# Optimization experiments

Hardware: AMD Instinct MI355X
Metric: run time of the kernel (lower is better)

Reference implementation:

```python
import jax, jax.numpy as jnp
import numpy as np

N_NODES = 100000
N_FEATS = 256
OUT_DIM = 64
NNZ_X = 1280000
N_EDGES = 1600000
KEEP_PROB = 0.9  # 1 - dropout_rate (dropout_rate = 0.1)


def setup_inputs() -> dict:
    key = jax.random.key(0)
    ks = jax.random.split(key, 7)
    feat_values = jax.random.normal(ks[0], (NNZ_X,), dtype=jnp.float32)
    feat_rows = jax.random.randint(ks[1], (NNZ_X,), 0, N_NODES, dtype=jnp.int32)
    feat_cols = jax.random.randint(ks[2], (NNZ_X,), 0, N_FEATS, dtype=jnp.int32)
    # GlorotNormal kernel: std = sqrt(2 / (fan_in + fan_out))
    glorot_std = float(np.sqrt(2.0 / (N_FEATS + OUT_DIM)))
    kernel = jax.random.normal(ks[3], (N_FEATS, OUT_DIM), dtype=jnp.float32) * glorot_std
    adj_values = jax.random.uniform(ks[4], (N_EDGES,), dtype=jnp.float32)
    adj_rows = jax.random.randint(ks[5], (N_EDGES,), 0, N_NODES, dtype=jnp.int32)
    adj_cols = jax.random.randint(ks[6], (N_EDGES,), 0, N_NODES, dtype=jnp.int32)
    return {
        "feat_values": feat_values,
        "kernel": kernel,
        "adj_values": adj_values,
        "feat_rows": feat_rows,
        "feat_cols": feat_cols,
        "adj_rows": adj_rows,
        "adj_cols": adj_cols,
    }


def reference(feat_values, kernel, adj_values, feat_rows, feat_cols, adj_rows, adj_cols):
    # sparse dropout on feature values (training=True path), deterministic key.
    # tf: keep = floor(keep_prob + U[0,1)) cast to bool; retain then scale 1/keep_prob
    u = jax.random.uniform(jax.random.key(42), feat_values.shape, dtype=feat_values.dtype)
    keep = jnp.floor(KEEP_PROB + u).astype(bool)
    v = jnp.where(keep, feat_values, jnp.zeros_like(feat_values)) * (1.0 / KEEP_PROB)

    # SpMM 1: XW[n, o] = sum_{(n,f) in X} v * kernel[f, o]
    xw = jax.ops.segment_sum(v[:, None] * kernel[feat_cols], feat_rows,
                             num_segments=N_NODES)  # [N, OUT]

    # SpMM 2: out[i, o] = sum_{(i,j) in A} a_ij * xw[j, o]
    agg = jax.ops.segment_sum(adj_values[:, None] * xw[adj_cols], adj_rows,
                              num_segments=N_NODES)  # [N, OUT]

    return jax.nn.relu(agg)
```

## Files before the change

kernel.cpp:

```cpp
#include <hip/hip_runtime.h>

#define N_NODES 100000
#define N_FEATS 256
#define OUT_DIM 64
#define NNZ_X   1280000
#define N_EDGES 1600000
#define NB      391
#define CHUNK   4096
#define KPT     8
#define CAPX    4352
#define CAPA    5120

__device__ __forceinline__ unsigned rotl32(unsigned x, unsigned d) {
    return (x << d) | (x >> (32u - d));
}

__device__ __forceinline__ float jax_uniform_42(unsigned e) {
    unsigned x0 = 0u, x1 = e;
    const unsigned ks0 = 0u, ks1 = 42u, ks2 = 0u ^ 42u ^ 0x1BD11BDAu;
    x0 += ks0; x1 += ks1;
#define TF_R(r) { x0 += x1; x1 = rotl32(x1, r); x1 ^= x0; }
    TF_R(13) TF_R(15) TF_R(26) TF_R(6)
    x0 += ks1; x1 += ks2 + 1u;
    TF_R(17) TF_R(29) TF_R(16) TF_R(24)
    x0 += ks2; x1 += ks0 + 2u;
    TF_R(13) TF_R(15) TF_R(26) TF_R(6)
    x0 += ks0; x1 += ks1 + 3u;
    TF_R(17) TF_R(29) TF_R(16) TF_R(24)
    x0 += ks1; x1 += ks2 + 4u;
    TF_R(13) TF_R(15) TF_R(26) TF_R(6)
    x0 += ks2; x1 += ks0 + 5u;
#undef TF_R
    unsigned bits = x0 ^ x1;
    return __uint_as_float((bits >> 9) | 0x3f800000u) - 1.0f;
}

__device__ __forceinline__ bool keep_42(unsigned e) {
    float u = jax_uniform_42(e);
    return floorf(0.9f + u) != 0.0f;
}

__device__ __forceinline__ unsigned short f32_bf16(float f) {
    unsigned bits = __float_as_uint(f);
    return (unsigned short)((bits + 0x7fffu + ((bits >> 16) & 1u)) >> 16);
}

__device__ __forceinline__ float bf16_f32(unsigned short u) {
    return __uint_as_float((unsigned)u << 16);
}

__global__ __launch_bounds__(512) void phase1(
        const float* __restrict__ fvals, const int* __restrict__ frows,
        const int* __restrict__ fcols,
        const float* __restrict__ avals, const int* __restrict__ arows,
        const int* __restrict__ acols,
        int* __restrict__ bcur_x, int* __restrict__ bcur_a,
        float2* __restrict__ gx, float2* __restrict__ ga) {
    const int isA = blockIdx.y;
    const float* vals = isA ? avals : fvals;
    const int* rows   = isA ? arows : frows;
    const int* cols   = isA ? acols : fcols;
    int* bcur         = isA ? bcur_a : bcur_x;
    float2* dst       = isA ? ga : gx;
    const unsigned cap = isA ? CAPA : CAPX;
    const unsigned n  = isA ? N_EDGES : NNZ_X;

    unsigned t = threadIdx.x;
    unsigned base = blockIdx.x * CHUNK;
    if (base >= n) return;

    __shared__ int cnt[512];
    __shared__ int start[512];
    __shared__ int cur[512];
    __shared__ int gbase[NB];
    __shared__ int s[256];
    __shared__ unsigned pArr[CHUNK];

    int rcache[KPT];

    cnt[t] = 0;
    __syncthreads();
    #pragma unroll
    for (int k = 0; k < KPT; k++) {
        unsigned i = base + k * 512u + t;
        int r = -1;
        if (i < n) {
            int rr = rows[i];
            if (isA || keep_42(i)) r = rr;
        }
        rcache[k] = r;
        if (r >= 0) atomicAdd(&cnt[(unsigned)r >> 8], 1);
    }
    __syncthreads();
    if (t < 256) s[t] = cnt[2*t] + cnt[2*t+1];
    __syncthreads();
    for (int off = 1; off < 256; off <<= 1) {
        int v = (t < 256u && t >= (unsigned)off) ? s[t - off] : 0;
        __syncthreads();
        if (t < 256u) s[t] += v;
        __syncthreads();
    }
    if (t < 256u) {
        int excl = t ? s[t-1] : 0;
        start[2*t]   = excl;
        start[2*t+1] = excl + cnt[2*t];
        cur[2*t]     = excl;
        cur[2*t+1]   = excl + cnt[2*t];
    }
    for (unsigned b = t; b < NB; b += 512u) {
        int cb = cnt[b];
        if (cb > 0) gbase[b] = atomicAdd(&bcur[b], cb);
    }
    __syncthreads();
    int n_valid = s[255];
    #pragma unroll
    for (int k = 0; k < KPT; k++) {
        int r = rcache[k];
        if (r >= 0) {
            unsigned b = (unsigned)r >> 8;
            int p = atomicAdd(&cur[b], 1);
            pArr[p] = (b << 20) | (((unsigned)r & 255u) << 12) | (k * 512u + t);
        }
    }
    __syncthreads();
    #pragma unroll
    for (int k = 0; k < KPT; k++) {
        int sidx = k * 512 + (int)t;
        if (sidx < n_valid) {
            unsigned m = pArr[sidx];
            unsigned b = m >> 20;
            unsigned rowlow = (m >> 12) & 255u;
            unsigned i = base + (m & 4095u);
            float v = vals[i];
            if (!isA) v *= (float)(1.0 / 0.9);
            unsigned packed = ((unsigned)cols[i] << 8) | rowlow;
            float2 e; e.x = v; e.y = __int_as_float((int)packed);
            dst[(size_t)b * cap + gbase[b] + (sidx - start[b])] = e;
        }
    }
}

__global__ __launch_bounds__(512) void sort_stage(
        const int* __restrict__ bcur_x, const float2* __restrict__ gx,
        const float* __restrict__ W, unsigned short* __restrict__ xw,
        const int* __restrict__ bcur_a, float2* __restrict__ ga,
        unsigned short* __restrict__ rs) {
    __shared__ float2 ent[CAPX];
    __shared__ int hist[256];
    __shared__ int starts[256];
    __shared__ int cursor[256];
    __shared__ int wtot[4];
    unsigned t = threadIdx.x;
    unsigned wid = t >> 6, lane = t & 63u;
    const int isA = (blockIdx.x >= NB);
    unsigned b = isA ? (blockIdx.x - NB) : blockIdx.x;

    if (!isA) {
        int cnt = bcur_x[b];
        const float2* src = gx + (size_t)b * CAPX;
        if (t < 256) hist[t] = 0;
        __syncthreads();
        for (int i = (int)t; i < cnt; i += 512)
            atomicAdd(&hist[((unsigned)__float_as_int(src[i].y)) & 255u], 1);
        __syncthreads();
        int inc = 0, binv = 0;
        if (wid < 4u) {
            unsigned bin = wid * 64u + lane;
            binv = hist[bin];
            inc = binv;
            #pragma unroll
            for (int d = 1; d < 64; d <<= 1) {
                int v = __shfl_up(inc, d, 64);
                if (lane >= (unsigned)d) inc += v;
            }
            if (lane == 63u) wtot[wid] = inc;
        }
        __syncthreads();
        if (wid < 4u) {
            int offw = 0;
            #pragma unroll
            for (int w = 0; w < 4; w++) if ((unsigned)w < wid) offw += wtot[w];
            unsigned bin = wid * 64u + lane;
            int excl = inc - binv + offw;
            starts[bin] = excl;
            cursor[bin] = excl;
        }
        __syncthreads();
        for (int i = (int)t; i < cnt; i += 512) {
            float2 e = src[i];
            int pos = atomicAdd(&cursor[((unsigned)__float_as_int(e.y)) & 255u], 1);
            ent[pos] = e;
        }
        __syncthreads();
        unsigned quarter = lane >> 4, sub = lane & 15u;
        const float4* W4 = (const float4*)W;
        ushort4* xw4 = (ushort4*)xw;
        for (unsigned r = wid; r < 256u; r += 8u) {
            int s0 = starts[r];
            int s1 = (r == 255u) ? cnt : starts[r + 1];
            float4 acc[4];
            #pragma unroll
            for (int j = 0; j < 4; j++) { acc[j].x = acc[j].y = acc[j].z = acc[j].w = 0.0f; }
            int p = s0;
            for (; p + 16 <= s1; p += 16) {
                float2 e[4];
                #pragma unroll
                for (int j = 0; j < 4; j++) e[j] = ent[p + 4 * quarter + j];
                float4 w[4];
                #pragma unroll
                for (int j = 0; j < 4; j++)
                    w[j] = W4[(((unsigned)__float_as_int(e[j].y)) >> 8) * 16u + sub];
                #pragma unroll
                for (int j = 0; j < 4; j++) {
                    acc[j].x = fmaf(e[j].x, w[j].x, acc[j].x);
                    acc[j].y = fmaf(e[j].x, w[j].y, acc[j].y);
                    acc[j].z = fmaf(e[j].x, w[j].z, acc[j].z);
                    acc[j].w = fmaf(e[j].x, w[j].w, acc[j].w);
                }
            }
            for (int q = p + (int)quarter; q < s1; q += 4) {
                float2 e = ent[q];
                float4 w = W4[(((unsigned)__float_as_int(e.y)) >> 8) * 16u + sub];
                acc[0].x = fmaf(e.x, w.x, acc[0].x);
                acc[0].y = fmaf(e.x, w.y, acc[0].y);
                acc[0].z = fmaf(e.x, w.z, acc[0].z);
                acc[0].w = fmaf(e.x, w.w, acc[0].w);
            }
            float ax = (acc[0].x + acc[1].x) + (acc[2].x + acc[3].x);
            float ay = (acc[0].y + acc[1].y) + (acc[2].y + acc[3].y);
            float az = (acc[0].z + acc[1].z) + (acc[2].z + acc[3].z);
            float aw = (acc[0].w + acc[1].w) + (acc[2].w + acc[3].w);
            ax += __shfl(ax, (int)(lane ^ 16u), 64);
            ay += __shfl(ay, (int)(lane ^ 16u), 64);
            az += __shfl(az, (int)(lane ^ 16u), 64);
            aw += __shfl(aw, (int)(lane ^ 16u), 64);
            ax += __shfl(ax, (int)(lane ^ 32u), 64);
            ay += __shfl(ay, (int)(lane ^ 32u), 64);
            az += __shfl(az, (int)(lane ^ 32u), 64);
            aw += __shfl(aw, (int)(lane ^ 32u), 64);
            unsigned grow = (b << 8) + r;
            if (quarter == 0 && grow < N_NODES) {
                ushort4 o;
                o.x = f32_bf16(ax); o.y = f32_bf16(ay);
                o.z = f32_bf16(az); o.w = f32_bf16(aw);
                xw4[(size_t)grow * 16u + sub] = o;
            }
        }
    } else {
        int cnt = bcur_a[b];
        float2* g = ga + (size_t)b * CAPA;
        if (t < 256) hist[t] = 0;
        __syncthreads();
        float2 ec[10];
        #pragma unroll
        for (int k = 0; k < 10; k++) {
            int i = k * 512 + (int)t;
            if (i < cnt) {
                float2 e = g[i];
                ec[k] = e;
                atomicAdd(&hist[((unsigned)__float_as_int(e.y)) & 255u], 1);
            }
        }
        __syncthreads();
        int inc = 0, binv = 0;
        if (wid < 4u) {
            unsigned bin = wid * 64u + lane;
            binv = hist[bin];
            inc = binv;
            #pragma unroll
            for (int d = 1; d < 64; d <<= 1) {
                int v = __shfl_up(inc, d, 64);
                if (lane >= (unsigned)d) inc += v;
            }
            if (lane == 63u) wtot[wid] = inc;
        }
        __syncthreads();
        if (wid < 4u) {
            int offw = 0;
            #pragma unroll
            for (int w = 0; w < 4; w++) if ((unsigned)w < wid) offw += wtot[w];
            unsigned bin = wid * 64u + lane;
            int excl = inc - binv + offw;
            cursor[bin] = excl;
            rs[(b << 8) + bin] = (unsigned short)excl;
        }
        __syncthreads();
        #pragma unroll
        for (int k = 0; k < 10; k++) {
            int i = k * 512 + (int)t;
            if (i < cnt) {
                unsigned packed = (unsigned)__float_as_int(ec[k].y);
                int pos = atomicAdd(&cursor[packed & 255u], 1);
                float2 o; o.x = ec[k].x; o.y = __int_as_float((int)(packed >> 8));
                g[pos] = o;
            }
        }
    }
}

__global__ void spmm2(const int* __restrict__ bcur_a,
                      const unsigned short* __restrict__ rs_a,
                      const float2* __restrict__ ga,
                      const unsigned short* __restrict__ xw,
                      float* __restrict__ out) {
    unsigned row  = blockIdx.x * 4u + (threadIdx.x >> 6);
    unsigned lane = threadIdx.x & 63u;
    if (row >= N_NODES) return;
    unsigned b = row >> 8, rl = row & 255u;
    int cnt = bcur_a[b];
    const float2* ent = ga + (size_t)b * CAPA;
    int s0 = rs_a[row];
    int s1 = (rl == 255u) ? cnt : (int)rs_a[row + 1];
    unsigned quarter = lane >> 4;
    unsigned sub     = lane & 15u;
    const ushort4* xw4 = (const ushort4*)xw;

    float4 acc[4];
    #pragma unroll
    for (int j = 0; j < 4; j++) { acc[j].x = acc[j].y = acc[j].z = acc[j].w = 0.0f; }
    int p = s0;
    for (; p + 16 <= s1; p += 16) {
        float2 e[4];
        #pragma unroll
        for (int j = 0; j < 4; j++) e[j] = ent[p + 4 * quarter + j];
        ushort4 u[4];
        #pragma unroll
        for (int j = 0; j < 4; j++)
            u[j] = xw4[((unsigned)__float_as_int(e[j].y)) * 16u + sub];
        #pragma unroll
        for (int j = 0; j < 4; j++) {
            acc[j].x = fmaf(e[j].x, bf16_f32(u[j].x), acc[j].x);
            acc[j].y = fmaf(e[j].x, bf16_f32(u[j].y), acc[j].y);
            acc[j].z = fmaf(e[j].x, bf16_f32(u[j].z), acc[j].z);
            acc[j].w = fmaf(e[j].x, bf16_f32(u[j].w), acc[j].w);
        }
    }
    for (int q = p + (int)quarter; q < s1; q += 4) {
        float2 e = ent[q];
        ushort4 u = xw4[((unsigned)__float_as_int(e.y)) * 16u + sub];
        acc[0].x = fmaf(e.x, bf16_f32(u.x), acc[0].x);
        acc[0].y = fmaf(e.x, bf16_f32(u.y), acc[0].y);
        acc[0].z = fmaf(e.x, bf16_f32(u.z), acc[0].z);
        acc[0].w = fmaf(e.x, bf16_f32(u.w), acc[0].w);
    }
    float ax = (acc[0].x + acc[1].x) + (acc[2].x + acc[3].x);
    float ay = (acc[0].y + acc[1].y) + (acc[2].y + acc[3].y);
    float az = (acc[0].z + acc[1].z) + (acc[2].z + acc[3].z);
    float aw = (acc[0].w + acc[1].w) + (acc[2].w + acc[3].w);
    ax += __shfl(ax, (int)(lane ^ 16u), 64);
    ay += __shfl(ay, (int)(lane ^ 16u), 64);
    az += __shfl(az, (int)(lane ^ 16u), 64);
    aw += __shfl(aw, (int)(lane ^ 16u), 64);
    ax += __shfl(ax, (int)(lane ^ 32u), 64);
    ay += __shfl(ay, (int)(lane ^ 32u), 64);
    az += __shfl(az, (int)(lane ^ 32u), 64);
    aw += __shfl(aw, (int)(lane ^ 32u), 64);
    if (quarter == 0) {
        float4 o;
        o.x = fmaxf(ax, 0.0f);
        o.y = fmaxf(ay, 0.0f);
        o.z = fmaxf(az, 0.0f);
        o.w = fmaxf(aw, 0.0f);
        ((float4*)out)[(size_t)row * 16u + sub] = o;
    }
}

extern "C" void kernel_launch(void* const* d_in, const int* in_sizes, int n_in,
                              void* d_out, int out_size, void* d_ws, size_t ws_size,
                              hipStream_t stream) {
    const float* feat_values = (const float*)d_in[0];
    const float* W           = (const float*)d_in[1];
    const float* adj_values  = (const float*)d_in[2];
    const int*   feat_rows   = (const int*)d_in[3];
    const int*   feat_cols   = (const int*)d_in[4];
    const int*   adj_rows    = (const int*)d_in[5];
    const int*   adj_cols    = (const int*)d_in[6];
    float* out = (float*)d_out;

    char* ws = (char*)d_ws;
    int* bcur_x = (int*)(ws + 0);
    int* bcur_a = (int*)(ws + 2048);
    unsigned short* rs_a = (unsigned short*)(ws + 4096);
    float2* gx  = (float2*)(ws + 204800);
    float2* ga  = (float2*)(ws + 13817856);
    unsigned short* xw = (unsigned short*)(ws + 29833216);

    hipMemsetAsync(ws, 0, 4096, stream);

    dim3 gp1((N_EDGES + CHUNK - 1) / CHUNK, 2);
    phase1<<<gp1, 512, 0, stream>>>(feat_values, feat_rows, feat_cols,
                                    adj_values, adj_rows, adj_cols,
                                    bcur_x, bcur_a, gx, ga);
    sort_stage<<<2 * NB, 512, 0, stream>>>(bcur_x, gx, W, xw, bcur_a, ga, rs_a);
    spmm2<<<(N_NODES + 3) / 4, 256, 0, stream>>>(bcur_a, rs_a, ga, xw, out);
}
```

Before: 209.9 us.

## Cache values/cols in phase1, wave-scan bins, widen spmm2 gathers to 16B

Phase1 now reads values and columns in the first pass and keeps them in registers, packing them into a 64-bit shared payload so the scatter pass no longer reissues random global reads. The 256-step shared-memory prefix scan with many barriers is replaced by a wave-level shuffle scan plus per-wave totals. spmm2 switches from 16 lanes of 8-byte bf16 gathers to 8 lanes of 16-byte gathers, with 8 edges processed in parallel per row. The trade is higher register use and a larger shared footprint in phase1 (64-bit payload plus bucket array).

```diff
diff --git a/kernel.cpp b/kernel.cpp
--- a/kernel.cpp
+++ b/kernel.cpp
@@ -49,6 +49,9 @@
     return __uint_as_float((unsigned)u << 16);
 }
 
+__device__ __forceinline__ float bflo(unsigned u) { return __uint_as_float(u << 16); }
+__device__ __forceinline__ float bfhi(unsigned u) { return __uint_as_float(u & 0xffff0000u); }
+
 __global__ __launch_bounds__(512) void phase1(
         const float* __restrict__ fvals, const int* __restrict__ frows,
         const int* __restrict__ fcols,
@@ -73,10 +76,14 @@
     __shared__ int start[512];
     __shared__ int cur[512];
     __shared__ int gbase[NB];
-    __shared__ int s[256];
-    __shared__ unsigned pArr[CHUNK];
-
-    int rcache[KPT];
+    __shared__ int wtot[8];
+    __shared__ int s_nvalid;
+    __shared__ unsigned long long payload[CHUNK];
+    __shared__ unsigned short bkt[CHUNK];
+
+    int   rcache[KPT];
+    float vcache[KPT];
+    int   ccache[KPT];
 
     cnt[t] = 0;
     __syncthreads();
@@ -86,40 +93,50 @@
         int r = -1;
         if (i < n) {
             int rr = rows[i];
-            if (isA || keep_42(i)) r = rr;
+            float v = vals[i];
+            int   c = cols[i];
+            if (isA || keep_42(i)) {
+                r = rr;
+                vcache[k] = isA ? v : v * (float)(1.0 / 0.9);
+                ccache[k] = c;
+            }
         }
         rcache[k] = r;
         if (r >= 0) atomicAdd(&cnt[(unsigned)r >> 8], 1);
     }
     __syncthreads();
-    if (t < 256) s[t] = cnt[2*t] + cnt[2*t+1];
+    unsigned lane = t & 63u, wid = t >> 6;
+    int binv = cnt[t];
+    int inc = binv;
+    #pragma unroll
+    for (int d = 1; d < 64; d <<= 1) {
+        int v = __shfl_up(inc, d, 64);
+        if (lane >= (unsigned)d) inc += v;
+    }
+    if (lane == 63u) wtot[wid] = inc;
     __syncthreads();
-    for (int off = 1; off < 256; off <<= 1) {
-        int v = (t < 256u && t >= (unsigned)off) ? s[t - off] : 0;
-        __syncthreads();
-        if (t < 256u) s[t] += v;
-        __syncthreads();
-    }
-    if (t < 256u) {
-        int excl = t ? s[t-1] : 0;
-        start[2*t]   = excl;
-        start[2*t+1] = excl + cnt[2*t];
-        cur[2*t]     = excl;
-        cur[2*t+1]   = excl + cnt[2*t];
-    }
-    for (unsigned b = t; b < NB; b += 512u) {
-        int cb = cnt[b];
-        if (cb > 0) gbase[b] = atomicAdd(&bcur[b], cb);
+    int offw = 0;
+    #pragma unroll
+    for (int w = 0; w < 8; w++) if ((unsigned)w < wid) offw += wtot[w];
+    int excl = offw + inc - binv;
+    start[t] = excl;
+    cur[t]   = excl;
+    if (t == 511u) s_nvalid = excl + binv;
+    if (t < NB) {
+        int cb = cnt[t];
+        if (cb > 0) gbase[t] = atomicAdd(&bcur[t], cb);
     }
     __syncthreads();
-    int n_valid = s[255];
+    int n_valid = s_nvalid;
     #pragma unroll
     for (int k = 0; k < KPT; k++) {
         int r = rcache[k];
         if (r >= 0) {
             unsigned b = (unsigned)r >> 8;
             int p = atomicAdd(&cur[b], 1);
-            pArr[p] = (b << 20) | (((unsigned)r & 255u) << 12) | (k * 512u + t);
+            unsigned packed = ((unsigned)ccache[k] << 8) | ((unsigned)r & 255u);
+            payload[p] = ((unsigned long long)__float_as_uint(vcache[k]) << 32) | packed;
+            bkt[p] = (unsigned short)b;
         }
     }
     __syncthreads();
@@ -127,14 +144,11 @@
     for (int k = 0; k < KPT; k++) {
         int sidx = k * 512 + (int)t;
         if (sidx < n_valid) {
-            unsigned m = pArr[sidx];
-            unsigned b = m >> 20;
-            unsigned rowlow = (m >> 12) & 255u;
-            unsigned i = base + (m & 4095u);
-            float v = vals[i];
-            if (!isA) v *= (float)(1.0 / 0.9);
-            unsigned packed = ((unsigned)cols[i] << 8) | rowlow;
-            float2 e; e.x = v; e.y = __int_as_float((int)packed);
+            unsigned b = bkt[sidx];
+            unsigned long long m = payload[sidx];
+            float2 e;
+            e.x = __uint_as_float((unsigned)(m >> 32));
+            e.y = __int_as_float((int)(unsigned)m);
             dst[(size_t)b * cap + gbase[b] + (sidx - start[b])] = e;
         }
     }
@@ -311,57 +325,70 @@
     const float2* ent = ga + (size_t)b * CAPA;
     int s0 = rs_a[row];
     int s1 = (rl == 255u) ? cnt : (int)rs_a[row + 1];
-    unsigned quarter = lane >> 4;
-    unsigned sub     = lane & 15u;
-    const ushort4* xw4 = (const ushort4*)xw;
-
-    float4 acc[4];
-    #pragma unroll
-    for (int j = 0; j < 4; j++) { acc[j].x = acc[j].y = acc[j].z = acc[j].w = 0.0f; }
-    int p = s0;
-    for (; p + 16 <= s1; p += 16) {
-        float2 e[4];
-        #pragma unroll
-        for (int j = 0; j < 4; j++) e[j] = ent[p + 4 * quarter + j];
-        ushort4 u[4];
-        #pragma unroll
-        for (int j = 0; j < 4; j++)
-            u[j] = xw4[((unsigned)__float_as_int(e[j].y)) * 16u + sub];
-        #pragma unroll
-        for (int j = 0; j < 4; j++) {
-            acc[j].x = fmaf(e[j].x, bf16_f32(u[j].x), acc[j].x);
-            acc[j].y = fmaf(e[j].x, bf16_f32(u[j].y), acc[j].y);
-            acc[j].z = fmaf(e[j].x, bf16_f32(u[j].z), acc[j].z);
-            acc[j].w = fmaf(e[j].x, bf16_f32(u[j].w), acc[j].w);
-        }
-    }
-    for (int q = p + (int)quarter; q < s1; q += 4) {
-        float2 e = ent[q];
-        ushort4 u = xw4[((unsigned)__float_as_int(e.y)) * 16u + sub];
-        acc[0].x = fmaf(e.x, bf16_f32(u.x), acc[0].x);
-        acc[0].y = fmaf(e.x, bf16_f32(u.y), acc[0].y);
-        acc[0].z = fmaf(e.x, bf16_f32(u.z), acc[0].z);
-        acc[0].w = fmaf(e.x, bf16_f32(u.w), acc[0].w);
-    }
-    float ax = (acc[0].x + acc[1].x) + (acc[2].x + acc[3].x);
-    float ay = (acc[0].y + acc[1].y) + (acc[2].y + acc[3].y);
-    float az = (acc[0].z + acc[1].z) + (acc[2].z + acc[3].z);
-    float aw = (acc[0].w + acc[1].w) + (acc[2].w + acc[3].w);
-    ax += __shfl(ax, (int)(lane ^ 16u), 64);
-    ay += __shfl(ay, (int)(lane ^ 16u), 64);
-    az += __shfl(az, (int)(lane ^ 16u), 64);
-    aw += __shfl(aw, (int)(lane ^ 16u), 64);
-    ax += __shfl(ax, (int)(lane ^ 32u), 64);
-    ay += __shfl(ay, (int)(lane ^ 32u), 64);
-    az += __shfl(az, (int)(lane ^ 32u), 64);
-    aw += __shfl(aw, (int)(lane ^ 32u), 64);
-    if (quarter == 0) {
-        float4 o;
-        o.x = fmaxf(ax, 0.0f);
-        o.y = fmaxf(ay, 0.0f);
-        o.z = fmaxf(az, 0.0f);
-        o.w = fmaxf(aw, 0.0f);
-        ((float4*)out)[(size_t)row * 16u + sub] = o;
+    unsigned oct = lane >> 3;
+    unsigned sub = lane & 7u;
+    const uint4* xw8 = (const uint4*)xw;
+
+    float acc[8];
+    #pragma unroll
+    for (int j = 0; j < 8; j++) acc[j] = 0.0f;
+
+    int p = s0 + (int)oct;
+    for (; p + 8 < s1; p += 16) {
+        float2 e0 = ent[p];
+        float2 e1 = ent[p + 8];
+        uint4 u0 = xw8[((unsigned)__float_as_int(e0.y)) * 8u + sub];
+        uint4 u1 = xw8[((unsigned)__float_as_int(e1.y)) * 8u + sub];
+        float v0 = e0.x, v1 = e1.x;
+        acc[0] = fmaf(v0, bflo(u0.x), acc[0]);
+        acc[1] = fmaf(v0, bfhi(u0.x), acc[1]);
+        acc[2] = fmaf(v0, bflo(u0.y), acc[2]);
+        acc[3] = fmaf(v0, bfhi(u0.y), acc[3]);
+        acc[4] = fmaf(v0, bflo(u0.z), acc[4]);
+        acc[5] = fmaf(v0, bfhi(u0.z), acc[5]);
+        acc[6] = fmaf(v0, bflo(u0.w), acc[6]);
+        acc[7] = fmaf(v0, bfhi(u0.w), acc[7]);
+        acc[0] = fmaf(v1, bflo(u1.x), acc[0]);
+        acc[1] = fmaf(v1, bfhi(u1.x), acc[1]);
+        acc[2] = fmaf(v1, bflo(u1.y), acc[2]);
+        acc[3] = fmaf(v1, bfhi(u1.y), acc[3]);
+        acc[4] = fmaf(v1, bflo(u1.z), acc[4]);
+        acc[5] = fmaf(v1, bfhi(u1.z), acc[5]);
+        acc[6] = fmaf(v1, bflo(u1.w), acc[6]);
+        acc[7] = fmaf(v1, bfhi(u1.w), acc[7]);
+    }
+    if (p < s1) {
+        float2 e = ent[p];
+        uint4 u = xw8[((unsigned)__float_as_int(e.y)) * 8u + sub];
+        float v = e.x;
+        acc[0] = fmaf(v, bflo(u.x), acc[0]);
+        acc[1] = fmaf(v, bfhi(u.x), acc[1]);
+        acc[2] = fmaf(v, bflo(u.y), acc[2]);
+        acc[3] = fmaf(v, bfhi(u.y), acc[3]);
+        acc[4] = fmaf(v, bflo(u.z), acc[4]);
+        acc[5] = fmaf(v, bfhi(u.z), acc[5]);
+        acc[6] = fmaf(v, bflo(u.w), acc[6]);
+        acc[7] = fmaf(v, bfhi(u.w), acc[7]);
+    }
+    #pragma unroll
+    for (int j = 0; j < 8; j++) {
+        acc[j] += __shfl_xor(acc[j], 8, 64);
+        acc[j] += __shfl_xor(acc[j], 16, 64);
+        acc[j] += __shfl_xor(acc[j], 32, 64);
+    }
+    if (oct == 0) {
+        float4 o0, o1;
+        o0.x = fmaxf(acc[0], 0.0f);
+        o0.y = fmaxf(acc[1], 0.0f);
+        o0.z = fmaxf(acc[2], 0.0f);
+        o0.w = fmaxf(acc[3], 0.0f);
+        o1.x = fmaxf(acc[4], 0.0f);
+        o1.y = fmaxf(acc[5], 0.0f);
+        o1.z = fmaxf(acc[6], 0.0f);
+        o1.w = fmaxf(acc[7], 0.0f);
+        float4* op = (float4*)(out + (size_t)row * 64u + sub * 8u);
+        op[0] = o0;
+        op[1] = o1;
     }
 }
 
```

Measured after the change: 184.3 us. 1.14x faster.
